# Kernel optimization log

Measured on AMD Instinct MI355X. Metric: run time of the kernel, lower is better.

Reference implementation:

```python
import jax, jax.numpy as jnp
import numpy as np

B, IN, HID, N, VAL, ONUM = 2048, 512, 256, 16, 400, 8
CH, CK = 4, 32            # comm heads, comm key/query size
CV = HID                  # comm_value_size forced to hidden_size
K_ACTIVE = 8              # top-k active units


def setup_inputs() -> dict:
    key = jax.random.key(0)
    ks = jax.random.split(key, 12)
    s = 0.02
    return dict(
        x=jax.random.normal(ks[0], (B, 1, IN), jnp.float32),
        hs=jax.random.normal(ks[1], (B, N, HID), jnp.float32),
        option=jax.random.normal(ks[2], (B, 2, ONUM), jnp.float32),
        value_w=jax.random.normal(ks[3], (IN, VAL), jnp.float32) * s,
        value_b=jnp.zeros((VAL,), jnp.float32),
        p_w=jax.random.normal(ks[4], (ONUM, N), jnp.float32),
        p_b=jax.random.normal(ks[5], (N,), jnp.float32),
        x2h_w=jax.random.normal(ks[6], (N, VAL, 3 * HID), jnp.float32) * s,
        h2h_w=jax.random.normal(ks[7], (N, HID, 3 * HID), jnp.float32) * s,
        q_w=jax.random.normal(ks[8], (N, HID, CH * CK), jnp.float32) * s,
        k_w=jax.random.normal(ks[9], (N, HID, CH * CK), jnp.float32) * s,
        v_w=jax.random.normal(ks[10], (N, HID, CH * CV), jnp.float32) * s,
        out_w=jax.random.normal(ks[11], (N, CH * CV, CV), jnp.float32) * s,
    )


def reference(x, hs, option, value_w, value_b, p_w, p_b, x2h_w, h2h_w, q_w, k_w, v_w, out_w):
    b = hs.shape[0]
    # --- input attention (null input appended) ---
    xcat = jnp.concatenate([x, jnp.zeros_like(x)], axis=1)          # (B,2,IN)
    value_layer = xcat @ value_w + value_b                          # (B,2,VAL), 1 input head -> mean is identity
    scores = jnp.einsum('bio,on->bni', option, p_w)                 # (B,N,2)
    p_bias = jnp.stack([jnp.broadcast_to(p_b, (b, N)),
                        jnp.zeros((b, N), x.dtype)], axis=2)        # (B,N,2)
    scores = scores + p_bias
    idx = jax.lax.top_k(scores[:, :, 0], K_ACTIVE)[1]               # (B,k)
    mask = jnp.zeros((b, N), x.dtype).at[jnp.arange(b)[:, None], idx].set(1.0)
    probs = jax.nn.softmax(scores, axis=-1)                         # dropout = identity (eval)
    inputs = jnp.matmul(probs, value_layer) * mask[:, :, None]      # (B,N,VAL)
    # --- grouped GRU ---
    gx = jnp.einsum('bnd,ndh->bnh', inputs, x2h_w)                  # (B,N,3H)
    gh = jnp.einsum('bnd,ndh->bnh', hs, h2h_w)
    i_r, i_i, i_n = jnp.split(gx, 3, axis=2)
    h_r, h_i, h_n = jnp.split(gh, 3, axis=2)
    reset = jax.nn.sigmoid(i_r + h_r)
    inp_g = jax.nn.sigmoid(i_i + h_i)
    newg = jnp.tanh(i_n + reset * h_n)
    hy = newg + inp_g * (hs - newg)                                 # (B,N,HID)
    # --- blocked_grad: identity fwd, grad*mask bwd ---
    m = mask[:, :, None]
    hb = m * hy + jax.lax.stop_gradient((1.0 - m) * hy)
    # --- communication attention ---
    def heads(t, d):  # (B,N,CH*d) -> (B,CH,N,d)
        return t.reshape(b, N, CH, d).transpose(0, 2, 1, 3)
    q = heads(jnp.einsum('bnd,ndh->bnh', hb, q_w), CK)
    k = heads(jnp.einsum('bnd,ndh->bnh', hb, k_w), CK)
    v = heads(jnp.einsum('bnd,ndh->bnh', hb, v_w), CV)
    att = jax.nn.softmax(jnp.einsum('bhnk,bhmk->bhnm', q, k) / (CK ** 0.5), axis=-1)
    att = att * mask[:, None, :, None]                              # mask query rows
    ctx = jnp.einsum('bhnm,bhmd->bhnd', att, v)                     # (B,CH,N,CV)
    ctx = ctx.transpose(0, 2, 1, 3).reshape(b, N, CH * CV)
    ctx = jnp.einsum('bnd,ndh->bnh', ctx, out_w) + hb               # residual
    return m * ctx + (1.0 - m) * hs
```

## Files before the change

### kernel.cpp

```cpp
#include <hip/hip_runtime.h>
#include <hip/hip_bf16.h>
#include <math.h>

#define BATCH 2048
#define INDIM 512
#define HID   256
#define NRIM  16
#define VAL   400
#define ONUM  8
#define CH    4
#define CK    32
#define CV    256
#define KACT  8
#define K2P   704

typedef __hip_bfloat16 hbf;
typedef __attribute__((ext_vector_type(8))) __bf16 bf16x8;
typedef __attribute__((ext_vector_type(4))) float f32x4;

__device__ __forceinline__ float fsig(float x) {
    x = fminf(fmaxf(x, -30.0f), 30.0f);
    return 1.0f / (1.0f + __expf(-x));
}
__device__ __forceinline__ float ftanh_(float x) {
    x = fminf(fmaxf(x, -15.0f), 15.0f);
    float e = __expf(2.0f * x);
    return (e - 1.0f) / (e + 1.0f);
}

__device__ __forceinline__ unsigned packbf(float a, float b) {
    hbf ha = __float2bfloat16(a), hb = __float2bfloat16(b);
    unsigned short ua, ub;
    __builtin_memcpy(&ua, &ha, 2);
    __builtin_memcpy(&ub, &hb, 2);
    return ((unsigned)ub << 16) | ua;
}

#define GLL(g, l) __builtin_amdgcn_global_load_lds(                                   \
    (const __attribute__((address_space(1))) void*)(g),                               \
    (__attribute__((address_space(3))) void*)(l), 16, 0, 0)

__device__ __forceinline__ void t_conv_body(
    const float* __restrict__ src, hbf* __restrict__ dst,
    int K, int C, long s_ns, long d_ns, int dstride,
    int koff, int coff, int cmode, int bx, int by, int bz, float* tileS)
{
    const int c0 = bx * 32, k0 = by * 32;
    const int t = threadIdx.x;
    float (*tile)[33] = (float(*)[33])tileS;
    const float* s = src + (size_t)bz * s_ns;

    {
        const int kr = t >> 3, cg = t & 7;
        const int k = k0 + kr, c = c0 + cg * 4;
        float4 v;
        if (k < K && c + 3 < C) {
            v = *(const float4*)(s + (size_t)k * C + c);
        } else {
            v.x = (k < K && c + 0 < C) ? s[(size_t)k * C + c + 0] : 0.0f;
            v.y = (k < K && c + 1 < C) ? s[(size_t)k * C + c + 1] : 0.0f;
            v.z = (k < K && c + 2 < C) ? s[(size_t)k * C + c + 2] : 0.0f;
            v.w = (k < K && c + 3 < C) ? s[(size_t)k * C + c + 3] : 0.0f;
        }
        tile[kr][cg * 4 + 0] = v.x;
        tile[kr][cg * 4 + 1] = v.y;
        tile[kr][cg * 4 + 2] = v.z;
        tile[kr][cg * 4 + 3] = v.w;
    }
    __syncthreads();
    {
        const int cr = t >> 3, kg = t & 7;
        const int c = c0 + cr;
        if (c < C) {
            const int cc = coff + (cmode ? (c < 512 ? c : c + 256) : c);
            hbf* drow = dst + (size_t)bz * d_ns + (size_t)cc * dstride + koff + k0 + kg * 4;
            float v0 = tile[kg * 4 + 0][cr];
            float v1 = tile[kg * 4 + 1][cr];
            float v2 = tile[kg * 4 + 2][cr];
            float v3 = tile[kg * 4 + 3][cr];
            *(uint2*)drow = make_uint2(packbf(v0, v1), packbf(v2, v3));
        }
    }
}

__global__ __launch_bounds__(256)
void mega_prep(const float* __restrict__ h2h_w, const float* __restrict__ x2h_w,
               const float* __restrict__ q_w, const float* __restrict__ k_w,
               const float* __restrict__ v_w, const float* __restrict__ out_w,
               const float* __restrict__ value_w, const float* __restrict__ option,
               const float* __restrict__ p_w, const float* __restrict__ p_b,
               const float* __restrict__ x,
               hbf* __restrict__ W2, hbf* __restrict__ Wqkv, hbf* __restrict__ Wout,
               hbf* __restrict__ Wv, float* __restrict__ p0g, float* __restrict__ maskg,
               hbf* __restrict__ xB)
{
    __shared__ float tileS[32 * 33];
    const int id = blockIdx.x;
    const int t  = threadIdx.x;

    if (id < 3072) {
        int l = id, bz = l / 192, rem = l % 192;
        t_conv_body(h2h_w, W2, 256, 768, 196608L, 720896L, K2P, 0, 0, 1,
                    rem % 24, rem / 24, bz, tileS);
    } else if (id < 8064) {
        int l = id - 3072, bz = l / 312, rem = l % 312;
        t_conv_body(x2h_w, W2, 400, 768, 307200L, 720896L, K2P, 256, 0, 0,
                    rem % 24, rem / 24, bz, tileS);
    } else if (id < 8576) {
        int l = id - 8064, bz = l / 32, rem = l % 32;
        t_conv_body(q_w, Wqkv, 256, 128, 32768L, 327680L, 256, 0, 0, 0,
                    rem % 4, rem / 4, bz, tileS);
    } else if (id < 9088) {
        int l = id - 8576, bz = l / 32, rem = l % 32;
        t_conv_body(k_w, Wqkv, 256, 128, 32768L, 327680L, 256, 0, 128, 0,
                    rem % 4, rem / 4, bz, tileS);
    } else if (id < 13184) {
        int l = id - 9088, bz = l / 256, rem = l % 256;
        t_conv_body(v_w, Wqkv, 256, 1024, 262144L, 327680L, 256, 0, 256, 0,
                    rem % 32, rem / 32, bz, tileS);
    } else if (id < 17280) {
        int l = id - 13184, bz = l / 256, rem = l % 256;
        t_conv_body(out_w, Wout, 1024, 256, 262144L, 262144L, 1024, 0, 0, 0,
                    rem % 8, rem / 8, bz, tileS);
    } else if (id < 17488) {
        int l = id - 17280;
        t_conv_body(value_w, Wv, 512, 400, 0L, 0L, 512, 0, 0, 0,
                    l % 13, l / 13, 0, tileS);
    } else if (id < 18672) {
        int l = id - 17488, n = l / 74, idx = (l % 74) * 256 + t;
        uint4 z; z.x = 0; z.y = 0; z.z = 0; z.w = 0;
        uint4* base = (uint4*)(W2 + (size_t)n * 720896);
        if (idx < 14336) {
            int c = 768 + idx / 56, u = 32 + idx % 56;
            base[(size_t)c * 88 + u] = z;
        } else {
            int i2 = idx - 14336;
            int c = i2 / 6, u = 82 + i2 % 6;
            base[(size_t)c * 88 + u] = z;
        }
    } else if (id < 18700) {
        int idx = (id - 18672) * 256 + t;
        int c = 400 + idx / 64, u = idx % 64;
        uint4 z; z.x = 0; z.y = 0; z.z = 0; z.w = 0;
        ((uint4*)Wv)[(size_t)c * 64 + u] = z;
    } else if (id < 19212) {
        int l = id - 18700, n = l / 32, idx = (l % 32) * 256 + t;
        int c = 512 + idx / 32, u = idx % 32;
        uint4 z; z.x = 0; z.y = 0; z.z = 0; z.w = 0;
        ((uint4*)(W2 + (size_t)n * 720896))[(size_t)c * 88 + u] = z;
    } else if (id < 19340) {
        const int bb = t >> 4, n = t & 15;
        const int b  = (id - 19212) * 16 + bb;
        float (*sc)[17] = (float(*)[17])tileS;
        float s0 = p_b[n], s1 = 0.0f;
        #pragma unroll
        for (int o = 0; o < ONUM; ++o) {
            s0 = fmaf(option[(b * 2 + 0) * ONUM + o], p_w[o * NRIM + n], s0);
            s1 = fmaf(option[(b * 2 + 1) * ONUM + o], p_w[o * NRIM + n], s1);
        }
        sc[bb][n] = s0;
        __syncthreads();
        int rank = 0;
        #pragma unroll
        for (int m = 0; m < NRIM; ++m) {
            float sm = sc[bb][m];
            if (sm > s0 || (sm == s0 && m < n)) rank++;
        }
        float mk = (rank < KACT) ? 1.0f : 0.0f;
        float mx = fmaxf(s0, s1);
        float e0 = __expf(s0 - mx), e1 = __expf(s1 - mx);
        p0g[b * NRIM + n]   = e0 / (e0 + e1);
        maskg[b * NRIM + n] = mk;
    } else {
        int i = (id - 19340) * 256 + t;
        float4 v = ((const float4*)x)[i];
        unsigned lo = packbf(v.x, v.y), hi = packbf(v.z, v.w);
        *(uint2*)(xB + (size_t)i * 4) = make_uint2(lo, hi);
    }
}

__global__ __launch_bounds__(256)
void k1b_a2(const float* __restrict__ hs, const float* __restrict__ vl0,
            const float* __restrict__ p0g, const float* __restrict__ maskg,
            const float* __restrict__ value_b, hbf* __restrict__ A2)
{
    const int b = blockIdx.x;
    const int t = threadIdx.x;
    __shared__ float vS[VAL], bS[VAL];
    __shared__ float p0S[16], mkS[16];
    if (t < 100) {
        ((float4*)vS)[t] = ((const float4*)(vl0 + (size_t)b * 512))[t];
        ((float4*)bS)[t] = ((const float4*)value_b)[t];
    }
    if (t >= 224 && t < 240) p0S[t - 224] = p0g[b * NRIM + (t - 224)];
    if (t >= 240)            mkS[t - 240] = maskg[b * NRIM + (t - 240)];
    __syncthreads();

    const size_t base = (size_t)b * NRIM;

    #pragma unroll
    for (int it = 0; it < 4; ++it) {
        int idx = it * 256 + t;
        int n = idx >> 6, j = idx & 63;
        float4 hv = ((const float4*)(hs + (base + n) * HID))[j];
        uint2 o = make_uint2(packbf(hv.x, hv.y), packbf(hv.z, hv.w));
        *(uint2*)(A2 + (base + n) * K2P + j * 4) = o;
    }

    for (int idx = t; idx < 1600; idx += 256) {
        int n = idx / 100, j = idx - n * 100;
        float p0 = p0S[n], mk = mkS[n];
        float4 v  = ((const float4*)vS)[j];
        float4 bb = ((const float4*)bS)[j];
        float a0 = mk * (p0 * v.x + (1.0f - p0) * bb.x);
        float a1 = mk * (p0 * v.y + (1.0f - p0) * bb.y);
        float a2 = mk * (p0 * v.z + (1.0f - p0) * bb.z);
        float a3 = mk * (p0 * v.w + (1.0f - p0) * bb.w);
        uint2 o = make_uint2(packbf(a0, a1), packbf(a2, a3));
        *(uint2*)(A2 + (base + n) * K2P + 256 + j * 4) = o;
    }

    if (t < 96) {
        int n = t / 6, j = t - n * 6;
        uint4 z; z.x = 0; z.y = 0; z.z = 0; z.w = 0;
        *(uint4*)(A2 + (base + n) * K2P + 656 + j * 8) = z;
    }
}

__device__ __forceinline__ void gemm_core64(const hbf* __restrict__ A, long lda,
                                            const hbf* __restrict__ B, long ldb,
                                            int K, short* As, short* Bs, f32x4 acc[4][4])
{
    const int t = threadIdx.x;
    const int w = t >> 6, lane = t & 63;
    const int l15 = lane & 15, l4 = lane >> 4;
    const int rl = lane >> 3;
    const int gu = (lane & 7) ^ rl;
    const int l7 = l15 & 7;

    const hbf* pa[4];
    const hbf* pb[4];
    #pragma unroll
    for (int q = 0; q < 4; ++q) {
        int row = q * 32 + w * 8 + rl;
        pa[q] = A + (size_t)row * lda + gu * 8;
        pb[q] = B + (size_t)row * ldb + gu * 8;
    }

    for (int kk = 0; kk < K; kk += 64) {
        __syncthreads();
        #pragma unroll
        for (int q = 0; q < 4; ++q) {
            GLL(pa[q], As + (q * 32 + w * 8) * 64);
            GLL(pb[q], Bs + (q * 32 + w * 8) * 64);
            pa[q] += 64; pb[q] += 64;
        }
        __syncthreads();

        const int wr = w >> 1, wc = w & 1;
        #pragma unroll
        for (int ks = 0; ks < 2; ++ks) {
            const int p = (ks * 4 + l4) ^ l7;
            bf16x8 af[4], bfr[4];
            #pragma unroll
            for (int m = 0; m < 4; ++m)
                af[m] = *(const bf16x8*)(As + (wr * 64 + m * 16 + l15) * 64 + p * 8);
            #pragma unroll
            for (int nb = 0; nb < 4; ++nb)
                bfr[nb] = *(const bf16x8*)(Bs + (wc * 64 + nb * 16 + l15) * 64 + p * 8);
            #pragma unroll
            for (int m = 0; m < 4; ++m)
                #pragma unroll
                for (int nb = 0; nb < 4; ++nb)
                    acc[m][nb] = __builtin_amdgcn_mfma_f32_16x16x32_bf16(af[m], bfr[nb], acc[m][nb], 0, 0, 0);
        }
    }
}

__global__ __launch_bounds__(256)
void k1v(const hbf* __restrict__ xB, const hbf* __restrict__ Wv,
         const float* __restrict__ value_b, float* __restrict__ vl0)
{
    __shared__ __align__(16) short As[128 * 64];
    __shared__ __align__(16) short Bs[128 * 64];
    const int m0 = (blockIdx.x >> 2) * 128;
    const int c0 = (blockIdx.x & 3) * 128;

    const hbf* A = xB + (size_t)m0 * INDIM;
    const hbf* B = Wv + (size_t)c0 * INDIM;

    f32x4 acc[4][4];
    f32x4 zz = {0.0f, 0.0f, 0.0f, 0.0f};
    #pragma unroll
    for (int m = 0; m < 4; ++m)
        #pragma unroll
        for (int nb = 0; nb < 4; ++nb) acc[m][nb] = zz;

    gemm_core64(A, INDIM, B, INDIM, INDIM, As, Bs, acc);

    const int t = threadIdx.x;
    const int w = t >> 6, lane = t & 63, l15 = lane & 15, l4 = lane >> 4;
    const int wr = w >> 1, wc = w & 1;
    #pragma unroll
    for (int nb = 0; nb < 4; ++nb) {
        int col = c0 + wc * 64 + nb * 16 + l15;
        float bias = (col < VAL) ? value_b[col] : 0.0f;
        #pragma unroll
        for (int m = 0; m < 4; ++m)
            #pragma unroll
            for (int j = 0; j < 4; ++j) {
                int row = m0 + wr * 64 + m * 16 + l4 * 4 + j;
                vl0[(size_t)row * 512 + col] = acc[m][nb][j] + bias;
            }
    }
}

__global__ __launch_bounds__(256)
void k2g(const hbf* __restrict__ A2, const hbf* __restrict__ W2, hbf* __restrict__ hyB)
{
    __shared__ __align__(16) short As[128 * 64];
    __shared__ __align__(16) short Bs[128 * 64];
    const int id = blockIdx.x;
    const int xcd = id & 7, idx = id >> 3;
    const int n  = xcd + ((idx >> 7) << 3);
    const int rem = idx & 127;
    const int m0 = (rem >> 3) * 128;
    const int c0 = rem & 7;

    const hbf* A = A2 + (size_t)n * K2P + (size_t)m0 * (NRIM * K2P);
    const hbf* Bb = W2 + (size_t)n * (1024 * K2P);

    const int t = threadIdx.x;
    const int w = t >> 6, lane = t & 63;
    const int l15 = lane & 15, l4 = lane >> 4;
    const int rl = lane >> 3;
    const int gu = (lane & 7) ^ rl;
    const int l7 = l15 & 7;
    const int wr = w >> 1, wc = w & 1;

    f32x4 acc[4][4];
    f32x4 zz = {0.0f, 0.0f, 0.0f, 0.0f};
    #pragma unroll
    for (int m = 0; m < 4; ++m)
        #pragma unroll
        for (int nb = 0; nb < 4; ++nb) acc[m][nb] = zz;

    const hbf* pa[4];
    const hbf* pb[4];
    int gq[4];
    #pragma unroll
    for (int q = 0; q < 4; ++q) {
        int row = q * 32 + w * 8 + rl;
        int wrow = ((row >> 4) & 3) * 256 + c0 * 32 + ((row >> 6) << 4) + (row & 15);
        pa[q] = A + (size_t)row * (NRIM * K2P) + gu * 8;
        pb[q] = Bb + (size_t)wrow * K2P + gu * 8;
        gq[q] = (2 * q + (w >> 1)) & 3;
    }

    for (int kk = 0; kk < 256; kk += 64) {
        __syncthreads();
        #pragma unroll
        for (int q = 0; q < 4; ++q) {
            GLL(pa[q], As + (q * 32 + w * 8) * 64);
            if (gq[q] != 2) GLL(pb[q], Bs + (q * 32 + w * 8) * 64);
            pa[q] += 64; pb[q] += 64;
        }
        __syncthreads();
        #pragma unroll
        for (int ks = 0; ks < 2; ++ks) {
            const int p = (ks * 4 + l4) ^ l7;
            bf16x8 af[4];
            #pragma unroll
            for (int m = 0; m < 4; ++m)
                af[m] = *(const bf16x8*)(As + (wr * 64 + m * 16 + l15) * 64 + p * 8);
            bf16x8 b0 = *(const bf16x8*)(Bs + (wc * 64 + 0 * 16 + l15) * 64 + p * 8);
            bf16x8 b1 = *(const bf16x8*)(Bs + (wc * 64 + 1 * 16 + l15) * 64 + p * 8);
            bf16x8 b3 = *(const bf16x8*)(Bs + (wc * 64 + 3 * 16 + l15) * 64 + p * 8);
            #pragma unroll
            for (int m = 0; m < 4; ++m) {
                acc[m][0] = __builtin_amdgcn_mfma_f32_16x16x32_bf16(af[m], b0, acc[m][0], 0, 0, 0);
                acc[m][1] = __builtin_amdgcn_mfma_f32_16x16x32_bf16(af[m], b1, acc[m][1], 0, 0, 0);
                acc[m][3] = __builtin_amdgcn_mfma_f32_16x16x32_bf16(af[m], b3, acc[m][3], 0, 0, 0);
            }
        }
    }

    for (int kk = 256; kk < K2P; kk += 64) {
        __syncthreads();
        #pragma unroll
        for (int q = 0; q < 4; ++q) {
            GLL(pa[q], As + (q * 32 + w * 8) * 64);
            if (gq[q] != 3) GLL(pb[q], Bs + (q * 32 + w * 8) * 64);
            pa[q] += 64; pb[q] += 64;
        }
        __syncthreads();
        #pragma unroll
        for (int ks = 0; ks < 2; ++ks) {
            const int p = (ks * 4 + l4) ^ l7;
            bf16x8 af[4];
            #pragma unroll
            for (int m = 0; m < 4; ++m)
                af[m] = *(const bf16x8*)(As + (wr * 64 + m * 16 + l15) * 64 + p * 8);
            bf16x8 b0 = *(const bf16x8*)(Bs + (wc * 64 + 0 * 16 + l15) * 64 + p * 8);
            bf16x8 b1 = *(const bf16x8*)(Bs + (wc * 64 + 1 * 16 + l15) * 64 + p * 8);
            bf16x8 b2 = *(const bf16x8*)(Bs + (wc * 64 + 2 * 16 + l15) * 64 + p * 8);
            #pragma unroll
            for (int m = 0; m < 4; ++m) {
                acc[m][0] = __builtin_amdgcn_mfma_f32_16x16x32_bf16(af[m], b0, acc[m][0], 0, 0, 0);
                acc[m][1] = __builtin_amdgcn_mfma_f32_16x16x32_bf16(af[m], b1, acc[m][1], 0, 0, 0);
                acc[m][2] = __builtin_amdgcn_mfma_f32_16x16x32_bf16(af[m], b2, acc[m][2], 0, 0, 0);
            }
        }
    }

    const int col = c0 * 32 + wc * 16 + l15;
    #pragma unroll
    for (int m = 0; m < 4; ++m)
        #pragma unroll
        for (int j = 0; j < 4; ++j) {
            int row = m0 + wr * 64 + m * 16 + l4 * 4 + j;
            size_t ridx = (size_t)row * NRIM + n;
            float reset = fsig(acc[m][0][j]);
            float inp   = fsig(acc[m][1][j]);
            float newg  = ftanh_(acc[m][2][j] + reset * acc[m][3][j]);
            float h     = __bfloat162float(A2[ridx * K2P + col]);
            hyB[ridx * HID + col] = __float2bfloat16(newg + inp * (h - newg));
        }
}

__global__ __launch_bounds__(256)
void k3g(const hbf* __restrict__ hyB, const hbf* __restrict__ Wqkv, hbf* __restrict__ qkv)
{
    __shared__ __align__(16) short As[128 * 64];
    __shared__ __align__(16) short Bs[128 * 64];
    const int id = blockIdx.x;
    const int xcd = id & 7, idx = id >> 3;
    const int n  = xcd + (idx / 160) * 8;
    const int rem = idx % 160;
    const int m0 = (rem / 10) * 128;
    const int c0 = (rem % 10) * 128;

    const hbf* A = hyB + (size_t)n * HID + (size_t)m0 * (NRIM * HID);
    const hbf* B = Wqkv + (size_t)n * (1280 * 256) + (size_t)c0 * 256;

    f32x4 acc[4][4];
    f32x4 zz = {0.0f, 0.0f, 0.0f, 0.0f};
    #pragma unroll
    for (int m = 0; m < 4; ++m)
        #pragma unroll
        for (int nb = 0; nb < 4; ++nb) acc[m][nb] = zz;

    gemm_core64(A, NRIM * HID, B, 256, 256, As, Bs, acc);

    const int t = threadIdx.x;
    const int w = t >> 6, lane = t & 63, l15 = lane & 15, l4 = lane >> 4;
    const int wr = w >> 1, wc = w & 1;
    #pragma unroll
    for (int m = 0; m < 4; ++m)
        #pragma unroll
        for (int nb = 0; nb < 4; ++nb) {
            int col = c0 + wc * 64 + nb * 16 + l15;
            int rb  = m0 + wr * 64 + m * 16 + l4 * 4;
            #pragma unroll
            for (int j = 0; j < 4; ++j)
                qkv[((size_t)(rb + j) * 16 + n) * 1280 + col] = __float2bfloat16(acc[m][nb][j]);
        }
}

__global__ __launch_bounds__(256)
void k4_attn(const hbf* __restrict__ qkv, const float* __restrict__ maskg,
             hbf* __restrict__ ctx)
{
    const int b = blockIdx.x;
    const int t = threadIdx.x;
    const int w = t >> 6, lane = t & 63;
    const int l15 = lane & 15, g = lane >> 4;

    __shared__ hbf vS[16 * 1024];

    {
        const int r = t >> 4, c = t & 15;
        const uint4* src = (const uint4*)(qkv + (size_t)(b * 16 + r) * 1280 + 256);
        uint4* dst = (uint4*)(vS + r * 1024);
        #pragma unroll
        for (int i = 0; i < 8; ++i) dst[c + i * 16] = src[c + i * 16];
    }

    const hbf* qrow = qkv + (size_t)(b * 16 + l15) * 1280 + w * 32 + g * 8;
    bf16x8 qf = *(const bf16x8*)(qrow);
    bf16x8 kf = *(const bf16x8*)(qrow + 128);
    f32x4 s = {0.f, 0.f, 0.f, 0.f};
    s = __builtin_amdgcn_mfma_f32_16x16x32_bf16(kf, qf, s, 0, 0, 0);

    const float scale = 0.17677669529663687f;
    float v0 = s[0] * scale, v1 = s[1] * scale, v2 = s[2] * scale, v3 = s[3] * scale;
    float mx = fmaxf(fmaxf(v0, v1), fmaxf(v2, v3));
    mx = fmaxf(mx, __shfl_xor(mx, 16));
    mx = fmaxf(mx, __shfl_xor(mx, 32));
    float e0 = __expf(v0 - mx), e1 = __expf(v1 - mx);
    float e2 = __expf(v2 - mx), e3 = __expf(v3 - mx);
    float sm = e0 + e1 + e2 + e3;
    sm += __shfl_xor(sm, 16);
    sm += __shfl_xor(sm, 32);
    float inv = maskg[b * NRIM + l15] / sm;

    unsigned u0 = packbf(e0 * inv, e1 * inv);
    unsigned u1 = packbf(e2 * inv, e3 * inv);
    int sl = l15 + (g << 5);
    unsigned f0 = __shfl((int)u0, sl);
    unsigned f1 = __shfl((int)u1, sl);
    unsigned f2 = __shfl((int)u0, sl + 16);
    unsigned f3 = __shfl((int)u1, sl + 16);
    if (lane >= 32) { f0 = 0; f1 = 0; f2 = 0; f3 = 0; }
    union { unsigned u[4]; bf16x8 v; } pf;
    pf.u[0] = f0; pf.u[1] = f1; pf.u[2] = f2; pf.u[3] = f3;

    __syncthreads();

    const unsigned short* vsu = (const unsigned short*)vS;
    const int vbase = (8 * (g & 1)) * 1024 + w * 256 + l15;
    hbf* crow = ctx + (size_t)(b * 16 + l15) * 1024 + w * 256 + g * 4;
    #pragma unroll
    for (int dc = 0; dc < 16; ++dc) {
        union { unsigned short u[8]; bf16x8 v; } vf;
        #pragma unroll
        for (int e = 0; e < 8; ++e)
            vf.u[e] = vsu[vbase + e * 1024 + dc * 16];
        f32x4 o = {0.f, 0.f, 0.f, 0.f};
        o = __builtin_amdgcn_mfma_f32_16x16x32_bf16(vf.v, pf.v, o, 0, 0, 0);
        unsigned lo = packbf(o[0], o[1]);
        unsigned hi = packbf(o[2], o[3]);
        *(uint2*)(crow + dc * 16) = make_uint2(lo, hi);
    }
}

__global__ __launch_bounds__(256)
void k5g(const hbf* __restrict__ ctx, const hbf* __restrict__ Wout,
         const hbf* __restrict__ hyB, const float* __restrict__ hs,
         const float* __restrict__ maskg, float* __restrict__ out)
{
    __shared__ __align__(16) short As[64 * 64];
    __shared__ __align__(16) short Bs[128 * 64];
    const int id = blockIdx.x;
    const int xcd = id & 7, idx = id >> 3;
    const int n  = xcd + ((idx >> 6) << 3);
    const int rem = idx & 63;
    const int m0 = (rem >> 1) * 64;
    const int c0 = (rem & 1) * 128;

    const int t = threadIdx.x;
    const int w = t >> 6, lane = t & 63;
    const int l15 = lane & 15, l4 = lane >> 4;
    const int rl = lane >> 3;
    const int gu = (lane & 7) ^ rl;
    const int l7 = l15 & 7;
    const int wr = w >> 1, wc = w & 1;

    const hbf* Bb = Wout + (size_t)n * (256 * 1024) + (size_t)c0 * 1024;

    const hbf* pa[2];
    #pragma unroll
    for (int q = 0; q < 2; ++q) {
        int b = m0 + q * 32 + w * 8 + rl;
        pa[q] = ctx + ((size_t)b * 16 + n) * 1024 + gu * 8;
    }
    const hbf* pb[4];
    #pragma unroll
    for (int q = 0; q < 4; ++q) {
        int row = q * 32 + w * 8 + rl;
        pb[q] = Bb + (size_t)row * 1024 + gu * 8;
    }

    f32x4 acc[2][4];
    f32x4 zz = {0.0f, 0.0f, 0.0f, 0.0f};
    #pragma unroll
    for (int m = 0; m < 2; ++m)
        #pragma unroll
        for (int nb = 0; nb < 4; ++nb) acc[m][nb] = zz;

    for (int kk = 0; kk < 1024; kk += 64) {
        __syncthreads();
        #pragma unroll
        for (int q = 0; q < 2; ++q) {
            GLL(pa[q], As + (q * 32 + w * 8) * 64);
            pa[q] += 64;
        }
        #pragma unroll
        for (int q = 0; q < 4; ++q) {
            GLL(pb[q], Bs + (q * 32 + w * 8) * 64);
            pb[q] += 64;
        }
        __syncthreads();
        #pragma unroll
        for (int ks = 0; ks < 2; ++ks) {
            const int p = (ks * 4 + l4) ^ l7;
            bf16x8 af[2], bfr[4];
            #pragma unroll
            for (int m = 0; m < 2; ++m)
                af[m] = *(const bf16x8*)(As + (wr * 32 + m * 16 + l15) * 64 + p * 8);
            #pragma unroll
            for (int nb = 0; nb < 4; ++nb)
                bfr[nb] = *(const bf16x8*)(Bs + (wc * 64 + nb * 16 + l15) * 64 + p * 8);
            #pragma unroll
            for (int m = 0; m < 2; ++m)
                #pragma unroll
                for (int nb = 0; nb < 4; ++nb)
                    acc[m][nb] = __builtin_amdgcn_mfma_f32_16x16x32_bf16(af[m], bfr[nb], acc[m][nb], 0, 0, 0);
        }
    }

    #pragma unroll
    for (int m = 0; m < 2; ++m)
        #pragma unroll
        for (int j = 0; j < 4; ++j) {
            int row = m0 + wr * 32 + m * 16 + l4 * 4 + j;
            float mk = maskg[row * NRIM + n];
            #pragma unroll
            for (int nb = 0; nb < 4; ++nb) {
                int col = c0 + wc * 64 + nb * 16 + l15;
                size_t idx2 = ((size_t)row * NRIM + n) * HID + col;
                out[idx2] = (mk > 0.5f) ? (acc[m][nb][j] + __bfloat162float(hyB[idx2]))
                                        : hs[idx2];
            }
        }
}

extern "C" void kernel_launch(void* const* d_in, const int* in_sizes, int n_in,
                              void* d_out, int out_size, void* d_ws, size_t ws_size,
                              hipStream_t stream) {
    const float* x       = (const float*)d_in[0];
    const float* hs      = (const float*)d_in[1];
    const float* option  = (const float*)d_in[2];
    const float* value_w = (const float*)d_in[3];
    const float* value_b = (const float*)d_in[4];
    const float* p_w     = (const float*)d_in[5];
    const float* p_b     = (const float*)d_in[6];
    const float* x2h_w   = (const float*)d_in[7];
    const float* h2h_w   = (const float*)d_in[8];
    const float* q_w     = (const float*)d_in[9];
    const float* k_w     = (const float*)d_in[10];
    const float* v_w     = (const float*)d_in[11];
    const float* out_w   = (const float*)d_in[12];
    float* out = (float*)d_out;

    char* ws = (char*)d_ws;
    hbf* A2   = (hbf*)(ws);
    hbf* ctx  = (hbf*)(ws);
    size_t off = 67108864;
    hbf* qkv  = (hbf*)(ws + off);
    off += 83886080;
    hbf* W2   = (hbf*)(ws + off); off += 23068672;
    hbf* Wqkv = (hbf*)(ws + off); off += 10485760;
    hbf* Wout = (hbf*)(ws + off); off += 8388608;
    hbf* hyB  = (hbf*)(ws + off); off += 16777216;
    float* vl0   = (float*)(ws + off); off += 4194304;
    hbf* xB   = (hbf*)(ws + off); off += 2097152;
    hbf* Wv   = (hbf*)(ws + off); off += 524288;
    float* p0g   = (float*)(ws + off); off += 131072;
    float* maskg = (float*)(ws + off); off += 131072;

    mega_prep<<<dim3(20364), dim3(256), 0, stream>>>(
        h2h_w, x2h_w, q_w, k_w, v_w, out_w, value_w, option, p_w, p_b, x,
        W2, Wqkv, Wout, Wv, p0g, maskg, xB);

    k1v<<<dim3(64), dim3(256), 0, stream>>>(xB, Wv, value_b, vl0);
    k1b_a2<<<dim3(BATCH), dim3(256), 0, stream>>>(hs, vl0, p0g, maskg, value_b, A2);

    k2g<<<dim3(2048), dim3(256), 0, stream>>>(A2, W2, hyB);

    k3g<<<dim3(2560), dim3(256), 0, stream>>>(hyB, Wqkv, qkv);

    k4_attn<<<dim3(BATCH), dim3(256), 0, stream>>>(qkv, maskg, ctx);

    k5g<<<dim3(1024), dim3(256), 0, stream>>>(ctx, Wout, hyB, hs, maskg, out);
}
```

Measured before the change: 203.1 us.

## Compact active rows per unit and skip x2h GEMM tiles for inactive rows

Adds a per-unit compaction kernel that builds a row list with mask-active batch rows first, followed by inactive rows. The GRU GEMM gathers A rows through this list and skips the x2h K-range for tiles made up only of inactive rows, whose input is zero after masking. About half the rows are inactive (top-8 of 16), so roughly half the x2h work can be skipped. The cost is an extra launch, indirect row loads, and a partially active tile at the boundary.

```diff
diff --git a/kernel.cpp b/kernel.cpp
--- a/kernel.cpp
+++ b/kernel.cpp
@@ -180,6 +180,43 @@
 }
 
 __global__ __launch_bounds__(256)
+void k_compact(const float* __restrict__ maskg, int* __restrict__ rowcnt,
+               int* __restrict__ rowlist)
+{
+    const int n = blockIdx.x;
+    const int t = threadIdx.x;
+    __shared__ int scan[256];
+    __shared__ int totalA;
+    int act[8];
+    int cnt = 0;
+    #pragma unroll
+    for (int i = 0; i < 8; ++i) {
+        int b = t * 8 + i;
+        act[i] = (maskg[b * NRIM + n] > 0.5f) ? 1 : 0;
+        cnt += act[i];
+    }
+    scan[t] = cnt;
+    __syncthreads();
+    for (int off = 1; off < 256; off <<= 1) {
+        int v = (t >= off) ? scan[t - off] : 0;
+        __syncthreads();
+        scan[t] += v;
+        __syncthreads();
+    }
+    if (t == 255) { totalA = scan[255]; rowcnt[n] = scan[255]; }
+    __syncthreads();
+    int aoff = scan[t] - cnt;
+    int ioff = totalA + (t * 8 - (scan[t] - cnt));
+    int* dst = rowlist + n * 2048;
+    #pragma unroll
+    for (int i = 0; i < 8; ++i) {
+        int b = t * 8 + i;
+        if (act[i]) dst[aoff++] = b;
+        else        dst[ioff++] = b;
+    }
+}
+
+__global__ __launch_bounds__(256)
 void k1b_a2(const float* __restrict__ hs, const float* __restrict__ vl0,
             const float* __restrict__ p0g, const float* __restrict__ maskg,
             const float* __restrict__ value_b, hbf* __restrict__ A2)
@@ -316,7 +353,9 @@
 }
 
 __global__ __launch_bounds__(256)
-void k2g(const hbf* __restrict__ A2, const hbf* __restrict__ W2, hbf* __restrict__ hyB)
+void k2g(const hbf* __restrict__ A2, const hbf* __restrict__ W2,
+         const int* __restrict__ rowcnt, const int* __restrict__ rowlist,
+         hbf* __restrict__ hyB)
 {
     __shared__ __align__(16) short As[128 * 64];
     __shared__ __align__(16) short Bs[128 * 64];
@@ -327,7 +366,10 @@
     const int m0 = (rem >> 3) * 128;
     const int c0 = rem & 7;
 
-    const hbf* A = A2 + (size_t)n * K2P + (size_t)m0 * (NRIM * K2P);
+    const int* rl_n = rowlist + n * 2048;
+    const int cntA  = rowcnt[n];
+    const bool skip2 = (m0 >= cntA);
+
     const hbf* Bb = W2 + (size_t)n * (1024 * K2P);
 
     const int t = threadIdx.x;
@@ -351,8 +393,9 @@
     #pragma unroll
     for (int q = 0; q < 4; ++q) {
         int row = q * 32 + w * 8 + rl;
+        int rb  = rl_n[m0 + row];
         int wrow = ((row >> 4) & 3) * 256 + c0 * 32 + ((row >> 6) << 4) + (row & 15);
-        pa[q] = A + (size_t)row * (NRIM * K2P) + gu * 8;
+        pa[q] = A2 + ((size_t)rb * NRIM + n) * K2P + gu * 8;
         pb[q] = Bb + (size_t)wrow * K2P + gu * 8;
         gq[q] = (2 * q + (w >> 1)) & 3;
     }
@@ -385,31 +428,33 @@
         }
     }
 
-    for (int kk = 256; kk < K2P; kk += 64) {
-        __syncthreads();
-        #pragma unroll
-        for (int q = 0; q < 4; ++q) {
-            GLL(pa[q], As + (q * 32 + w * 8) * 64);
-            if (gq[q] != 3) GLL(pb[q], Bs + (q * 32 + w * 8) * 64);
-            pa[q] += 64; pb[q] += 64;
-        }
-        __syncthreads();
-        #pragma unroll
-        for (int ks = 0; ks < 2; ++ks) {
-            const int p = (ks * 4 + l4) ^ l7;
-            bf16x8 af[4];
-            #pragma unroll
-            for (int m = 0; m < 4; ++m)
-                af[m] = *(const bf16x8*)(As + (wr * 64 + m * 16 + l15) * 64 + p * 8);
-            bf16x8 b0 = *(const bf16x8*)(Bs + (wc * 64 + 0 * 16 + l15) * 64 + p * 8);
-            bf16x8 b1 = *(const bf16x8*)(Bs + (wc * 64 + 1 * 16 + l15) * 64 + p * 8);
-            bf16x8 b2 = *(const bf16x8*)(Bs + (wc * 64 + 2 * 16 + l15) * 64 + p * 8);
-            #pragma unroll
-            for (int m = 0; m < 4; ++m) {
-                acc[m][0] = __builtin_amdgcn_mfma_f32_16x16x32_bf16(af[m], b0, acc[m][0], 0, 0, 0);
-                acc[m][1] = __builtin_amdgcn_mfma_f32_16x16x32_bf16(af[m], b1, acc[m][1], 0, 0, 0);
-                acc[m][2] = __builtin_amdgcn_mfma_f32_16x16x32_bf16(af[m], b2, acc[m][2], 0, 0, 0);
+    if (!skip2) {
+        for (int kk = 256; kk < K2P; kk += 64) {
+            __syncthreads();
+            #pragma unroll
+            for (int q = 0; q < 4; ++q) {
+                GLL(pa[q], As + (q * 32 + w * 8) * 64);
+                if (gq[q] != 3) GLL(pb[q], Bs + (q * 32 + w * 8) * 64);
+                pa[q] += 64; pb[q] += 64;
             }
+            __syncthreads();
+            #pragma unroll
+            for (int ks = 0; ks < 2; ++ks) {
+                const int p = (ks * 4 + l4) ^ l7;
+                bf16x8 af[4];
+                #pragma unroll
+                for (int m = 0; m < 4; ++m)
+                    af[m] = *(const bf16x8*)(As + (wr * 64 + m * 16 + l15) * 64 + p * 8);
+                bf16x8 b0 = *(const bf16x8*)(Bs + (wc * 64 + 0 * 16 + l15) * 64 + p * 8);
+                bf16x8 b1 = *(const bf16x8*)(Bs + (wc * 64 + 1 * 16 + l15) * 64 + p * 8);
+                bf16x8 b2 = *(const bf16x8*)(Bs + (wc * 64 + 2 * 16 + l15) * 64 + p * 8);
+                #pragma unroll
+                for (int m = 0; m < 4; ++m) {
+                    acc[m][0] = __builtin_amdgcn_mfma_f32_16x16x32_bf16(af[m], b0, acc[m][0], 0, 0, 0);
+                    acc[m][1] = __builtin_amdgcn_mfma_f32_16x16x32_bf16(af[m], b1, acc[m][1], 0, 0, 0);
+                    acc[m][2] = __builtin_amdgcn_mfma_f32_16x16x32_bf16(af[m], b2, acc[m][2], 0, 0, 0);
+                }
+            }
         }
     }
 
@@ -418,8 +463,9 @@
     for (int m = 0; m < 4; ++m)
         #pragma unroll
         for (int j = 0; j < 4; ++j) {
-            int row = m0 + wr * 64 + m * 16 + l4 * 4 + j;
-            size_t ridx = (size_t)row * NRIM + n;
+            int i   = m0 + wr * 64 + m * 16 + l4 * 4 + j;
+            int rb  = rl_n[i];
+            size_t ridx = (size_t)rb * NRIM + n;
             float reset = fsig(acc[m][0][j]);
             float inp   = fsig(acc[m][1][j]);
             float newg  = ftanh_(acc[m][2][j] + reset * acc[m][3][j]);
@@ -658,15 +704,19 @@
     hbf* Wv   = (hbf*)(ws + off); off += 524288;
     float* p0g   = (float*)(ws + off); off += 131072;
     float* maskg = (float*)(ws + off); off += 131072;
+    int* rowcnt  = (int*)(ws + off);   off += 256;
+    int* rowlist = (int*)(ws + off);   off += 131072;
 
     mega_prep<<<dim3(20364), dim3(256), 0, stream>>>(
         h2h_w, x2h_w, q_w, k_w, v_w, out_w, value_w, option, p_w, p_b, x,
         W2, Wqkv, Wout, Wv, p0g, maskg, xB);
 
+    k_compact<<<dim3(NRIM), dim3(256), 0, stream>>>(maskg, rowcnt, rowlist);
+
     k1v<<<dim3(64), dim3(256), 0, stream>>>(xB, Wv, value_b, vl0);
     k1b_a2<<<dim3(BATCH), dim3(256), 0, stream>>>(hs, vl0, p0g, maskg, value_b, A2);
 
-    k2g<<<dim3(2048), dim3(256), 0, stream>>>(A2, W2, hyB);
+    k2g<<<dim3(2048), dim3(256), 0, stream>>>(A2, W2, rowcnt, rowlist, hyB);
 
     k3g<<<dim3(2560), dim3(256), 0, stream>>>(hyB, Wqkv, qkv);
 
```

New measurement: 211.6 us. 1.04x slower.
